# Kernel tuning notes

Hardware: AMD Instinct MI355X
Metric: run time of the kernel (lower is better)

## Reference

```python
import jax, jax.numpy as jnp
import numpy as np

B, N1, D, H = 64, 201, 128, 4
HALF = (N1 - 1) // 2  # 100 pickup/delivery pairs
V_RANGE = 6.0
NEG = -1e20


def _uni(key, shape):
    s = 1.0 / np.sqrt(shape[-1])
    return jax.random.uniform(key, shape, jnp.float32, -s, s)


def setup_inputs() -> dict:
    key = jax.random.key(0)
    ks = jax.random.split(key, 24)
    h_wave = jax.random.normal(ks[0], (B, N1, D), jnp.float32)
    # solution must be a valid permutation per batch (it is argsorted / self-gathered)
    solution = jax.vmap(lambda k: jax.random.permutation(k, N1))(jax.random.split(ks[1], B)).astype(jnp.int32)
    selection_recent = jax.random.uniform(ks[2], (B, 4, HALF), jnp.float32)
    pre_action = jax.random.randint(ks[3], (B, 2), 1, HALF).astype(jnp.int32)
    mask_table = jnp.zeros((B, N1, N1), dtype=bool)
    params = dict(
        Wn=_uni(ks[4], (D, D)), Wg=_uni(ks[5], (D, D)),
        rm_WQ=_uni(ks[6], (H, D, D)), rm_WK=_uni(ks[7], (H, D, D)),
        rm_w1=_uni(ks[8], (2 * H + 4, 32)), rm_b1=_uni(ks[9], (32,)),
        rm_w2=_uni(ks[10], (32, 32)), rm_b2=_uni(ks[11], (32,)),
        rm_w3=_uni(ks[12], (32, 1)), rm_b3=_uni(ks[13], (1,)),
        i1_Wq=_uni(ks[14], (H, D, D)), i1_Wk=_uni(ks[15], (H, D, D)),
        i2_Wq=_uni(ks[16], (H, D, D)), i2_Wk=_uni(ks[17], (H, D, D)),
        re_w1=_uni(ks[18], (4 * H, 32)), re_b1=_uni(ks[19], (32,)),
        re_w2=_uni(ks[20], (32, 32)), re_b2=_uni(ks[21], (32,)),
        re_w3=_uni(ks[22], (32, 1)), re_b3=_uni(ks[23], (1,)),
    )
    return dict(h_wave=h_wave, solution=solution, selection_recent=selection_recent,
                pre_action=pre_action, mask_table=mask_table, **params)


def _mlp(x, w1, b1, w2, b2, w3, b3):
    x = jax.nn.relu(x @ w1 + b1)
    x = jax.nn.relu(x @ w2 + b2)
    return (x @ w3 + b3)[..., 0]


def _mha_compat(q, k, Wq, Wk):
    # q: [B,Q,Din], k: [B,K,Din]; Wq/Wk: [H,Din,Dh] -> compat [H,B,Q,K]
    Q = jnp.einsum('bqd,hde->hbqe', q, Wq)
    K = jnp.einsum('bkd,hde->hbke', k, Wk)
    return jnp.einsum('hbqe,hbke->hbqk', Q, K) * (1.0 / np.sqrt(Wq.shape[-1]))


def _removal(h_hat, solution, selection_recent, WQ, WK, w1, b1, w2, b2, w3, b3):
    pre = jnp.argsort(solution, axis=1)
    post = jnp.take_along_axis(solution, solution, axis=1)
    hQ = jnp.einsum('bnd,hde->hbne', h_hat, WQ)  # [H,B,N1,D]
    hK = jnp.einsum('bnd,hde->hbne', h_hat, WK)
    Qpre = jnp.take_along_axis(hQ, pre[None, :, :, None], axis=2)
    Kpost = jnp.take_along_axis(hK, post[None, :, :, None], axis=2)
    comp = ((Qpre * hK).sum(-1) + (hQ * Kpost).sum(-1) - (Qpre * Kpost).sum(-1))[:, :, 1:]  # [H,B,N1-1]
    pairing = jnp.concatenate([comp[:, :, :N1 // 2], comp[:, :, N1 // 2:]], axis=0)  # [2H,B,HALF]
    feat = jnp.concatenate([jnp.transpose(pairing, (1, 2, 0)),
                            jnp.transpose(selection_recent, (0, 2, 1))], axis=-1)  # [B,HALF,2H+4]
    return _mlp(feat, w1, b1, w2, b2, w3, b3)  # [B,HALF]


def _reinsertion(h_hat, pos_pickup, pos_delivery, solution, Wq1, Wk1, Wq2, Wk2, w1, b1, w2, b2, w3, b3):
    ar = jnp.arange(B)
    h_p = h_hat[ar, pos_pickup][:, None, :]   # [B,1,D]
    h_d = h_hat[ar, pos_delivery][:, None, :]
    h_nb = jnp.take_along_axis(h_hat, solution[:, :, None], axis=1)  # [B,N1,D]

    def as_row(c):  # [H,B,1,N1] -> [B,N1,1,H] broadcast over columns
        return jnp.broadcast_to(jnp.transpose(c, (1, 2, 3, 0)).reshape(B, N1, 1, H), (B, N1, N1, H))

    def as_col(c):  # [H,B,1,N1] -> [B,1,N1,H] broadcast over rows
        return jnp.broadcast_to(jnp.transpose(c, (1, 2, 3, 0)).reshape(B, 1, N1, H), (B, N1, N1, H))

    feat = jnp.concatenate([
        as_row(_mha_compat(h_p, h_hat, Wq1, Wk1)),
        as_row(_mha_compat(h_p, h_nb, Wq2, Wk2)),
        as_col(_mha_compat(h_d, h_hat, Wq1, Wk1)),
        as_col(_mha_compat(h_d, h_nb, Wq2, Wk2)),
    ], axis=-1)  # [B,N1,N1,4H]
    return _mlp(feat, w1, b1, w2, b2, w3, b3)  # [B,N1,N1]


def _forward(h_wave, selection_recent, Wn, Wg, rm_WQ, rm_WK, rm_w1, rm_b1, rm_w2, rm_b2,
             rm_w3, rm_b3, i1_Wq, i1_Wk, i2_Wq, i2_Wk, re_w1, re_b1, re_w2, re_b2,
             re_w3, re_b3, solution, pre_action, mask_table):
    ar = jnp.arange(B)
    h_hat = h_wave @ Wn + (jnp.max(h_wave, axis=1) @ Wg)[:, None, :]
    t1 = jnp.tanh(_removal(h_hat, solution, selection_recent, rm_WQ, rm_WK,
                           rm_w1, rm_b1, rm_w2, rm_b2, rm_w3, rm_b3)) * V_RANGE
    t1 = jnp.where(pre_action[0, 0] > 0, t1.at[ar, pre_action[:, 0]].set(NEG), t1)
    logp1 = jax.nn.log_softmax(t1, axis=-1)
    a1 = jnp.argmax(t1, axis=-1)  # deterministic stand-in for Categorical sampling
    ll1 = jnp.take_along_axis(logp1, a1[:, None], axis=1)[:, 0]
    pos_pickup = 1 + a1
    pos_delivery = pos_pickup + HALF
    t2 = jnp.tanh(_reinsertion(h_hat, pos_pickup, pos_delivery, solution,
                               i1_Wq, i1_Wk, i2_Wq, i2_Wk,
                               re_w1, re_b1, re_w2, re_b2, re_w3, re_b3)) * V_RANGE
    t2 = jnp.where(mask_table, NEG, t2).reshape(B, N1 * N1)
    logp2 = jax.nn.log_softmax(t2, axis=-1)
    pair = jnp.argmax(t2, axis=-1)
    ll2 = jnp.take_along_axis(logp2, pair[:, None], axis=1)[:, 0]
    action = jnp.stack([a1, pair // N1, pair % N1], axis=-1)
    return action, ll1 + ll2


def reference(h_wave, solution, selection_recent, pre_action, mask_table,
              Wn, Wg, rm_WQ, rm_WK, rm_w1, rm_b1, rm_w2, rm_b2, rm_w3, rm_b3,
              i1_Wq, i1_Wk, i2_Wq, i2_Wk, re_w1, re_b1, re_w2, re_b2, re_w3, re_b3):
    return _forward(h_wave, selection_recent, Wn, Wg, rm_WQ, rm_WK, rm_w1, rm_b1,
                    rm_w2, rm_b2, rm_w3, rm_b3, i1_Wq, i1_Wk, i2_Wq, i2_Wk,
                    re_w1, re_b1, re_w2, re_b2, re_w3, re_b3,
                    solution, pre_action, mask_table)
```

## Files before the change

### kernel.cpp

```cpp
#include <hip/hip_runtime.h>
#include <math.h>

#define BB 64
#define N1 201
#define DD 128
#define HALF 100
#define NN (N1*N1)
#define NEGV (-1e20f)
#define QSCALE 0.08838834764831845f
#define NELE 1646592u

typedef __attribute__((ext_vector_type(8))) short short8v;
typedef __attribute__((ext_vector_type(4))) float float4v;

#define OFF_M    0u
#define OFF_MF   196608u
#define OFF_HWB  516096u
#define OFF_HHAT 2985984u
#define OFF_HBF  4632576u
#define OFF_G    7102464u
#define OFF_CMP  7110656u
#define OFF_Q    7161856u
#define OFF_ROWH 7292928u
#define OFF_COLH 7704576u
#define OFF_SC   8116224u
#define OFF_PM   8116480u
#define OFF_PS   8120576u
#define OFF_PI   8124672u
#define OFF_W2F  8128768u

__device__ __forceinline__ unsigned short f2bf(float x) {
    unsigned u = __float_as_uint(x);
    unsigned r = u + 0x7fffu + ((u >> 16) & 1u);
    return (unsigned short)(r >> 16);
}
__device__ __forceinline__ float bf2f(unsigned short h) {
    return __uint_as_float(((unsigned)h) << 16);
}

__global__ void kprep2(const float* __restrict__ rmWQ, const float* __restrict__ rmWK,
                       const float* __restrict__ i1Wq, const float* __restrict__ i1Wk,
                       const float* __restrict__ i2Wq, const float* __restrict__ i2Wk,
                       float* __restrict__ ws) {
    int m = blockIdx.x, ig = blockIdx.y, jg = blockIdx.z, t = threadIdx.x;
    const float* WQ; const float* WK;
    if (m < 4)      { WQ = rmWQ + m*16384;     WK = rmWK + m*16384; }
    else if (m < 8) { WQ = i1Wq + (m-4)*16384; WK = i1Wk + (m-4)*16384; }
    else            { WQ = i2Wq + (m-8)*16384; WK = i2Wk + (m-8)*16384; }
    __shared__ float wq[32*132];
    __shared__ float wk[32*133];
    for (int idx = t; idx < 32*128; idx += 128) {
        int r = idx >> 7, e = idx & 127;
        wq[r*132 + e] = WQ[(ig*32 + r)*128 + e];
        wk[r*133 + e] = WK[(jg*32 + r)*128 + e];
    }
    __syncthreads();
    int j = t & 31, iq = t >> 5;
    #pragma unroll
    for (int i2 = 0; i2 < 8; ++i2) {
        int i = iq*8 + i2;
        float acc = 0.f;
        #pragma unroll 8
        for (int e = 0; e < 128; ++e) acc += wq[i*132 + e]*wk[j*133 + e];
        ws[OFF_M + m*16384 + (ig*32 + i)*128 + jg*32 + j] = acc;
    }
}

__global__ void kfrag(const float* __restrict__ Wn, const float* __restrict__ re_w2,
                      float* __restrict__ ws) {
    int bid = blockIdx.x;
    int l = threadIdx.x;
    if (bid == 416) {
        unsigned short* w2f = (unsigned short*)(ws + OFF_W2F);
        for (int idx = l; idx < 2048; idx += 64) {
            int fs = idx >> 9, ll = (idx >> 3) & 63, i = idx & 7;
            int j = 16*(fs >> 1) + (ll & 15);
            int k = ((ll >> 4)*8) + i;
            float v = re_w2[k*32 + j];
            unsigned short hi = f2bf(v);
            w2f[idx] = (fs & 1) ? f2bf(v - bf2f(hi)) : hi;
        }
        return;
    }
    int mat = bid >> 5, rem = bid & 31, nt = rem >> 2, ks = rem & 3;
    const float* src = (mat < 12) ? (ws + OFF_M + mat*16384) : Wn;
    unsigned short* mf = (unsigned short*)(ws + OFF_MF)
                       + (size_t)mat*49152 + (size_t)((nt*4 + ks)*3)*512 + l*8;
    #pragma unroll
    for (int i = 0; i < 8; ++i) {
        int k = ks*32 + (l >> 4)*8 + i;
        int col = nt*16 + (l & 15);
        float v = src[k*128 + col];
        unsigned short h = f2bf(v);
        float r1 = v - bf2f(h);
        unsigned short mm = f2bf(r1);
        unsigned short lo = f2bf(r1 - bf2f(mm));
        mf[i] = h; mf[512 + i] = mm; mf[1024 + i] = lo;
    }
}

__global__ void khw3(const float* __restrict__ hw, float* __restrict__ ws) {
    unsigned idx = blockIdx.x*256u + threadIdx.x;
    if (idx >= NELE) return;
    unsigned short* hh = (unsigned short*)(ws + OFF_HWB);
    unsigned short* hm = hh + NELE;
    unsigned short* hl = hh + 2u*NELE;
    float v = hw[idx];
    unsigned short a = f2bf(v);
    float r1 = v - bf2f(a);
    unsigned short b = f2bf(r1);
    unsigned short c = f2bf(r1 - bf2f(b));
    hh[idx] = a; hm[idx] = b; hl[idx] = c;
}

__global__ void khmaxg2(const float* __restrict__ hw, const float* __restrict__ Wg,
                        float* __restrict__ g) {
    int b = blockIdx.x, d = threadIdx.x;
    __shared__ float hm[128];
    float m = -INFINITY;
    const float* src = hw + (size_t)b*N1*DD + d;
    for (int n = 0; n < N1; ++n) m = fmaxf(m, src[n*DD]);
    hm[d] = m;
    __syncthreads();
    float acc = 0.f;
    for (int k = 0; k < 128; ++k) acc += hm[k] * Wg[k*128 + d];
    g[b*128 + d] = acc;
}

__global__ __launch_bounds__(256) void khhat2(const float* __restrict__ g,
                                              float* __restrict__ ws) {
    int b = blockIdx.x, cg = blockIdx.y;
    int t = threadIdx.x, w = t >> 6, l = t & 63;
    const unsigned short* hwh = (const unsigned short*)(ws + OFF_HWB);
    const unsigned short* hwm = hwh + NELE;
    const unsigned short* hwl = hwh + 2u*NELE;
    const unsigned short* wnf = (const unsigned short*)(ws + OFF_MF) + (size_t)12*49152;
    float* hhat = ws + OFF_HHAT;
    unsigned short* hbh = (unsigned short*)(ws + OFF_HBF);
    unsigned short* hbm = hbh + NELE;
    unsigned short* hbl = hbh + 2u*NELE;
    int col0 = cg*32 + (l & 15);
    float g0 = g[b*128 + col0];
    float g1 = g[b*128 + col0 + 16];
    for (int mt = w; mt < 13; mt += 4) {
        int arow = mt*16 + (l & 15); if (arow > 200) arow = 200;
        size_t abase = ((size_t)b*N1 + arow)*DD;
        float4v acc0 = {g0, g0, g0, g0};
        float4v acc1 = {g1, g1, g1, g1};
        #pragma unroll
        for (int ks = 0; ks < 4; ++ks) {
            size_t ao = abase + ks*32 + (l >> 4)*8;
            short8v ah = *(const short8v*)(hwh + ao);
            short8v am = *(const short8v*)(hwm + ao);
            short8v al = *(const short8v*)(hwl + ao);
            const short8v* bf0 = (const short8v*)(wnf + (size_t)(((cg*2 + 0)*4 + ks)*3)*512) + l;
            const short8v* bf1 = (const short8v*)(wnf + (size_t)(((cg*2 + 1)*4 + ks)*3)*512) + l;
            short8v bh0 = bf0[0], bm0 = bf0[64], bl0 = bf0[128];
            short8v bh1 = bf1[0], bm1 = bf1[64], bl1 = bf1[128];
            acc0 = __builtin_amdgcn_mfma_f32_16x16x32_bf16(ah, bh0, acc0, 0, 0, 0);
            acc1 = __builtin_amdgcn_mfma_f32_16x16x32_bf16(ah, bh1, acc1, 0, 0, 0);
            acc0 = __builtin_amdgcn_mfma_f32_16x16x32_bf16(ah, bm0, acc0, 0, 0, 0);
            acc1 = __builtin_amdgcn_mfma_f32_16x16x32_bf16(ah, bm1, acc1, 0, 0, 0);
            acc0 = __builtin_amdgcn_mfma_f32_16x16x32_bf16(am, bh0, acc0, 0, 0, 0);
            acc1 = __builtin_amdgcn_mfma_f32_16x16x32_bf16(am, bh1, acc1, 0, 0, 0);
            acc0 = __builtin_amdgcn_mfma_f32_16x16x32_bf16(ah, bl0, acc0, 0, 0, 0);
            acc1 = __builtin_amdgcn_mfma_f32_16x16x32_bf16(ah, bl1, acc1, 0, 0, 0);
            acc0 = __builtin_amdgcn_mfma_f32_16x16x32_bf16(al, bh0, acc0, 0, 0, 0);
            acc1 = __builtin_amdgcn_mfma_f32_16x16x32_bf16(al, bh1, acc1, 0, 0, 0);
            acc0 = __builtin_amdgcn_mfma_f32_16x16x32_bf16(am, bm0, acc0, 0, 0, 0);
            acc1 = __builtin_amdgcn_mfma_f32_16x16x32_bf16(am, bm1, acc1, 0, 0, 0);
        }
        #pragma unroll
        for (int r = 0; r < 4; ++r) {
            int row = mt*16 + (l >> 4)*4 + r;
            if (row < N1) {
                size_t i0 = ((size_t)b*N1 + row)*DD + col0;
                float v0 = acc0[r], v1 = acc1[r];
                hhat[i0] = v0; hhat[i0 + 16] = v1;
                unsigned short a0 = f2bf(v0); float r10 = v0 - bf2f(a0);
                unsigned short b0 = f2bf(r10);
                hbh[i0] = a0; hbm[i0] = b0; hbl[i0] = f2bf(r10 - bf2f(b0));
                unsigned short a1 = f2bf(v1); float r11 = v1 - bf2f(a1);
                unsigned short b1 = f2bf(r11);
                hbh[i0+16] = a1; hbm[i0+16] = b1; hbl[i0+16] = f2bf(r11 - bf2f(b1));
            }
        }
    }
}

__global__ __launch_bounds__(256) void kAC(const int* __restrict__ solution,
                                           float* __restrict__ ws) {
    int b = blockIdx.x, h = blockIdx.y;
    int t = threadIdx.x, w = t >> 6, l = t & 63;
    __shared__ float As[N1*132];
    __shared__ int sol[N1], pre[N1], post[N1];
    if (t < N1) sol[t] = solution[b*N1 + t];
    __syncthreads();
    if (t < N1) { pre[sol[t]] = t; post[t] = sol[sol[t]]; }
    const unsigned short* hbh = (const unsigned short*)(ws + OFF_HBF);
    const unsigned short* hbm = hbh + NELE;
    const unsigned short* hbl = hbh + 2u*NELE;
    const unsigned short* mfm = (const unsigned short*)(ws + OFF_MF) + (size_t)h*49152;
    for (int mt = 0; mt < 13; ++mt) {
        int arow = mt*16 + (l & 15); if (arow > 200) arow = 200;
        size_t abase = ((size_t)b*N1 + arow)*DD;
        float4v acc0 = {0.f, 0.f, 0.f, 0.f};
        float4v acc1 = {0.f, 0.f, 0.f, 0.f};
        #pragma unroll
        for (int ks = 0; ks < 4; ++ks) {
            size_t ao = abase + ks*32 + (l >> 4)*8;
            short8v ah = *(const short8v*)(hbh + ao);
            short8v am = *(const short8v*)(hbm + ao);
            short8v al = *(const short8v*)(hbl + ao);
            const short8v* bf0 = (const short8v*)(mfm + (size_t)(((2*w + 0)*4 + ks)*3)*512) + l;
            const short8v* bf1 = (const short8v*)(mfm + (size_t)(((2*w + 1)*4 + ks)*3)*512) + l;
            short8v bh0 = bf0[0], bm0 = bf0[64], bl0 = bf0[128];
            short8v bh1 = bf1[0], bm1 = bf1[64], bl1 = bf1[128];
            acc0 = __builtin_amdgcn_mfma_f32_16x16x32_bf16(ah, bh0, acc0, 0, 0, 0);
            acc1 = __builtin_amdgcn_mfma_f32_16x16x32_bf16(ah, bh1, acc1, 0, 0, 0);
            acc0 = __builtin_amdgcn_mfma_f32_16x16x32_bf16(ah, bm0, acc0, 0, 0, 0);
            acc1 = __builtin_amdgcn_mfma_f32_16x16x32_bf16(ah, bm1, acc1, 0, 0, 0);
            acc0 = __builtin_amdgcn_mfma_f32_16x16x32_bf16(am, bh0, acc0, 0, 0, 0);
            acc1 = __builtin_amdgcn_mfma_f32_16x16x32_bf16(am, bh1, acc1, 0, 0, 0);
            acc0 = __builtin_amdgcn_mfma_f32_16x16x32_bf16(ah, bl0, acc0, 0, 0, 0);
            acc1 = __builtin_amdgcn_mfma_f32_16x16x32_bf16(ah, bl1, acc1, 0, 0, 0);
            acc0 = __builtin_amdgcn_mfma_f32_16x16x32_bf16(al, bh0, acc0, 0, 0, 0);
            acc1 = __builtin_amdgcn_mfma_f32_16x16x32_bf16(al, bh1, acc1, 0, 0, 0);
            acc0 = __builtin_amdgcn_mfma_f32_16x16x32_bf16(am, bm0, acc0, 0, 0, 0);
            acc1 = __builtin_amdgcn_mfma_f32_16x16x32_bf16(am, bm1, acc1, 0, 0, 0);
        }
        #pragma unroll
        for (int r = 0; r < 4; ++r) {
            int row = mt*16 + (l >> 4)*4 + r;
            if (row < N1) {
                int col = 2*w*16 + (l & 15);
                As[row*132 + col] = acc0[r];
                As[row*132 + col + 16] = acc1[r];
            }
        }
    }
    __syncthreads();
    const float2* X = (const float2*)(ws + OFF_HHAT) + (size_t)b*N1*64;
    float* cmp = ws + OFF_CMP + (h*64 + b)*200;
    for (int n = 1 + w; n <= 200; n += 4) {
        int pn = pre[n], po = post[n];
        float2 xn = X[n*64 + l], xp = X[po*64 + l];
        float2 ap = *(const float2*)&As[pn*132 + 2*l];
        float2 an = *(const float2*)&As[n*132 + 2*l];
        float v = ap.x*(xn.x - xp.x) + ap.y*(xn.y - xp.y) + an.x*xp.x + an.y*xp.y;
        #pragma unroll
        for (int off = 32; off; off >>= 1) v += __shfl_xor(v, off);
        if (l == 0) cmp[n - 1] = v;
    }
}

__global__ void krmq(const float* __restrict__ sel, const int* __restrict__ pre_action,
                     const float* __restrict__ w1, const float* __restrict__ b1,
                     const float* __restrict__ w2, const float* __restrict__ b2,
                     const float* __restrict__ w3, const float* __restrict__ b3,
                     const float* __restrict__ Mall, const float* __restrict__ hhat,
                     const float* __restrict__ cmpg, float* __restrict__ sc,
                     float* __restrict__ q) {
    int b = blockIdx.x, t = threadIdx.x;
    __shared__ float t1l[100];
    __shared__ int ppd[2];
    __shared__ float xp[128], xd[128];
    if (t < 100) {
        float f[12];
        #pragma unroll
        for (int h = 0; h < 4; ++h) {
            f[h]     = cmpg[(h*64 + b)*200 + t];
            f[4 + h] = cmpg[(h*64 + b)*200 + 100 + t];
        }
        #pragma unroll
        for (int s = 0; s < 4; ++s) f[8 + s] = sel[b*400 + s*100 + t];
        float h1[32];
        #pragma unroll
        for (int k = 0; k < 32; ++k) h1[k] = b1[k];
        #pragma unroll
        for (int j = 0; j < 12; ++j) {
            const float* wr = w1 + j*32;
            #pragma unroll
            for (int k = 0; k < 32; ++k) h1[k] += f[j]*wr[k];
        }
        #pragma unroll
        for (int k = 0; k < 32; ++k) h1[k] = fmaxf(h1[k], 0.f);
        float acc[32];
        #pragma unroll
        for (int j = 0; j < 32; ++j) acc[j] = b2[j];
        #pragma unroll
        for (int k = 0; k < 32; ++k) {
            const float* wr = w2 + k*32;
            #pragma unroll
            for (int j = 0; j < 32; ++j) acc[j] += h1[k]*wr[j];
        }
        float out = b3[0];
        #pragma unroll
        for (int j = 0; j < 32; ++j) out += fmaxf(acc[j], 0.f)*w3[j];
        t1l[t] = tanhf(out)*6.0f;
    }
    __syncthreads();
    if (t == 0) {
        if (pre_action[0] > 0) t1l[pre_action[b*2]] = NEGV;
        float M = -INFINITY; int a1 = 0;
        for (int i = 0; i < 100; ++i) if (t1l[i] > M) { M = t1l[i]; a1 = i; }
        float S = 0.f;
        for (int i = 0; i < 100; ++i) S += __expf(t1l[i] - M);
        int* ia = (int*)sc;
        ia[b] = a1;
        sc[192 + b] = -__logf(S);
        ppd[0] = 1 + a1; ppd[1] = 101 + a1;
    }
    __syncthreads();
    int pp = ppd[0], pd = ppd[1];
    const float* hb = hhat + (size_t)b*N1*DD;
    xp[t] = hb[pp*DD + t];
    xd[t] = hb[pd*DD + t];
    __syncthreads();
    int j = t;
    #pragma unroll
    for (int h = 0; h < 4; ++h) {
        const float* M1 = Mall + (4 + h)*16384;
        const float* M2 = Mall + (8 + h)*16384;
        float a1p = 0, a2p = 0, a1d = 0, a2d = 0;
        for (int i = 0; i < 128; ++i) {
            float w1v = M1[i*128 + j], w2v = M2[i*128 + j];
            a1p += xp[i]*w1v; a1d += xd[i]*w1v;
            a2p += xp[i]*w2v; a2d += xd[i]*w2v;
        }
        q[((0*4 + h)*64 + b)*128 + j] = a1p*QSCALE;
        q[((1*4 + h)*64 + b)*128 + j] = a2p*QSCALE;
        q[((2*4 + h)*64 + b)*128 + j] = a1d*QSCALE;
        q[((3*4 + h)*64 + b)*128 + j] = a2d*QSCALE;
    }
}

__global__ void krowcol(const int* __restrict__ solution, const float* __restrict__ w1,
                        const float* __restrict__ b1, const float* __restrict__ qg,
                        const float* __restrict__ hhat, float* __restrict__ rowH,
                        float* __restrict__ colH) {
    int b = blockIdx.x, ch = blockIdx.y, t = threadIdx.x;
    int n = ch*51 + t;
    int ne = ch*51 + 51; if (ne > N1) ne = N1;
    if (n >= ne || t >= 51) return;
    int sn = solution[b*N1 + n];
    const float* ra = hhat + ((size_t)b*N1 + n)*DD;
    const float* rb = hhat + ((size_t)b*N1 + sn)*DD;
    float cv[16];
    #pragma unroll
    for (int j = 0; j < 16; ++j) cv[j] = 0.f;
    for (int ec = 0; ec < 4; ++ec) {
        float xa[32], xb[32];
        #pragma unroll
        for (int q4 = 0; q4 < 8; ++q4) {
            float4 va = ((const float4*)(ra + ec*32))[q4];
            float4 vb = ((const float4*)(rb + ec*32))[q4];
            xa[q4*4+0]=va.x; xa[q4*4+1]=va.y; xa[q4*4+2]=va.z; xa[q4*4+3]=va.w;
            xb[q4*4+0]=vb.x; xb[q4*4+1]=vb.y; xb[q4*4+2]=vb.z; xb[q4*4+3]=vb.w;
        }
        #pragma unroll
        for (int j = 0; j < 16; ++j) {
            const float* qp = qg + ((size_t)j*64 + b)*128 + ec*32;
            int kind = j >> 2;
            float a = 0.f;
            if (kind & 1) {
                #pragma unroll
                for (int e = 0; e < 32; ++e) a += qp[e]*xb[e];
            } else {
                #pragma unroll
                for (int e = 0; e < 32; ++e) a += qp[e]*xa[e];
            }
            cv[j] += a;
        }
    }
    float* rO = rowH + ((size_t)b*N1 + n)*32;
    float* cO = colH + ((size_t)b*N1 + n)*32;
    #pragma unroll
    for (int k = 0; k < 32; ++k) {
        float rh = b1[k], chh = 0.f;
        #pragma unroll
        for (int j = 0; j < 8; ++j)  rh  += cv[j]*w1[j*32 + k];
        #pragma unroll
        for (int j = 8; j < 16; ++j) chh += cv[j]*w1[j*32 + k];
        rO[k] = rh; cO[k] = chh;
    }
}

__global__ __launch_bounds__(64) void kt2(
        const unsigned char* __restrict__ maskt,
        const float* __restrict__ rowH, const float* __restrict__ colH,
        const unsigned short* __restrict__ w2f,
        const float* __restrict__ b2g, const float* __restrict__ w3g,
        const float* __restrict__ b3g,
        float* __restrict__ pm, float* __restrict__ ps, int* __restrict__ pi) {
    int b = blockIdx.x, cy = blockIdx.y, rz = blockIdx.z;
    int l = threadIdx.x;
    int c0 = cy*64;
    int r0 = rz*13, rend = r0 + 13; if (rend > N1) rend = N1;
    int rcnt = rend - r0;
    __shared__ float colc[64*36];
    __shared__ float rowr[13*36];

    const short8v* wf = (const short8v*)w2f;
    short8v w2hi0 = wf[0*64 + l];
    short8v w2lo0 = wf[1*64 + l];
    short8v w2hi1 = wf[2*64 + l];
    short8v w2lo1 = wf[3*64 + l];
    int sg = l >> 4;
    float4v b2f0 = *(const float4v*)(b2g + sg*4);
    float4v b2f1 = *(const float4v*)(b2g + 16 + sg*4);
    float4v w3f0 = *(const float4v*)(w3g + sg*4);
    float4v w3f1 = *(const float4v*)(w3g + 16 + sg*4);
    float b3v = b3g[0];

    {
        int cg = c0 + l;
        float4v* dst = (float4v*)(colc + l*36);
        if (cg < N1) {
            const float4v* src = (const float4v*)(colH + ((size_t)b*N1 + cg)*32);
            #pragma unroll
            for (int q = 0; q < 8; ++q) dst[q] = src[q];
        } else {
            float4v z = {0.f, 0.f, 0.f, 0.f};
            #pragma unroll
            for (int q = 0; q < 8; ++q) dst[q] = z;
        }
    }
    for (int idx = l; idx < rcnt*32; idx += 64) {
        int rr = idx >> 5, k = idx & 31;
        rowr[rr*36 + k] = rowH[((size_t)b*N1 + r0 + rr)*32 + k];
    }
    __syncthreads();

    float m = -INFINITY, s = 0.f;
    int mi = 0x7fffffff;
    int c = c0 + l;
    bool valid = c < N1;
    const unsigned char* mrow = maskt + (size_t)b*NN + c0 + l;

    union U8 { unsigned u[4]; short8v s8; };

    for (int rr = 0; rr < rcnt; ++rr) {
        int r = r0 + rr;
        const float4v* rp = (const float4v*)(rowr + rr*36 + sg*8);
        float4v ra = rp[0], rb = rp[1];
        float outv = 0.f;
        #pragma unroll
        for (int g = 0; g < 4; ++g) {
            const float4v* cp = (const float4v*)(colc + (16*g + (l & 15))*36 + sg*8);
            float4v ca = cp[0], cb = cp[1];
            float h[8];
            #pragma unroll
            for (int e = 0; e < 4; ++e) {
                h[e]   = fmaxf(ra[e] + ca[e], 0.f);
                h[4+e] = fmaxf(rb[e] + cb[e], 0.f);
            }
            U8 B, L;
            #pragma unroll
            for (int e = 0; e < 4; ++e) {
                unsigned ph, pl;
                asm("v_cvt_pk_bf16_f32 %0, %1, %2" : "=v"(ph) : "v"(h[2*e]), "v"(h[2*e+1]));
                float h0 = __uint_as_float(ph << 16);
                float h1f = __uint_as_float(ph & 0xffff0000u);
                float l0 = h[2*e] - h0, l1 = h[2*e+1] - h1f;
                asm("v_cvt_pk_bf16_f32 %0, %1, %2" : "=v"(pl) : "v"(l0), "v"(l1));
                B.u[e] = ph; L.u[e] = pl;
            }
            short8v bh = B.s8, bl = L.s8;
            float4v a0 = b2f0, a1 = b2f1;
            a0 = __builtin_amdgcn_mfma_f32_16x16x32_bf16(w2hi0, bh, a0, 0, 0, 0);
            a0 = __builtin_amdgcn_mfma_f32_16x16x32_bf16(w2hi0, bl, a0, 0, 0, 0);
            a0 = __builtin_amdgcn_mfma_f32_16x16x32_bf16(w2lo0, bh, a0, 0, 0, 0);
            a0 = __builtin_amdgcn_mfma_f32_16x16x32_bf16(w2lo0, bl, a0, 0, 0, 0);
            a1 = __builtin_amdgcn_mfma_f32_16x16x32_bf16(w2hi1, bh, a1, 0, 0, 0);
            a1 = __builtin_amdgcn_mfma_f32_16x16x32_bf16(w2hi1, bl, a1, 0, 0, 0);
            a1 = __builtin_amdgcn_mfma_f32_16x16x32_bf16(w2lo1, bh, a1, 0, 0, 0);
            a1 = __builtin_amdgcn_mfma_f32_16x16x32_bf16(w2lo1, bl, a1, 0, 0, 0);
            float p = 0.f;
            #pragma unroll
            for (int reg = 0; reg < 4; ++reg) {
                p += fmaxf(a0[reg], 0.f)*w3f0[reg];
                p += fmaxf(a1[reg], 0.f)*w3f1[reg];
            }
            p += __shfl_xor(p, 16);
            p += __shfl_xor(p, 32);
            if (sg == g) outv = p + b3v;
        }
        float ex = __expf(2.f*outv);
        float tv = 6.f - 12.f/(ex + 1.f);
        if (mrow[(size_t)r*N1]) tv = NEGV;
        if (valid) {
            if (tv > m) { s = s*__expf(m - tv) + 1.f; m = tv; mi = r*N1 + c; }
            else        { s += __expf(tv - m); }
        }
    }
    #pragma unroll
    for (int off = 1; off < 64; off <<= 1) {
        float om = __shfl_xor(m, off);
        float os = __shfl_xor(s, off);
        int oi = __shfl_xor(mi, off);
        float M2 = fmaxf(m, om);
        float sn = (s > 0.f ? s*__expf(m - M2) : 0.f)
                 + (os > 0.f ? os*__expf(om - M2) : 0.f);
        int in_;
        if (m > om) in_ = mi; else if (om > m) in_ = oi; else in_ = (mi < oi ? mi : oi);
        m = M2; s = sn; mi = in_;
    }
    if (l == 0) {
        int slot = b*64 + cy*16 + rz;
        pm[slot] = m; ps[slot] = s; pi[slot] = mi;
    }
}

__global__ void kfinal(float* __restrict__ out, const float* __restrict__ pm,
                       const float* __restrict__ ps, const int* __restrict__ pi,
                       const float* __restrict__ sc) {
    int b = blockIdx.x, lane = threadIdx.x;
    float m = pm[b*64 + lane];
    float s = ps[b*64 + lane];
    int mi = pi[b*64 + lane];
    #pragma unroll
    for (int off = 1; off < 64; off <<= 1) {
        float om = __shfl_xor(m, off);
        float os = __shfl_xor(s, off);
        int oi = __shfl_xor(mi, off);
        float M2 = fmaxf(m, om);
        float sn = (s > 0.f ? s*__expf(m - M2) : 0.f)
                 + (os > 0.f ? os*__expf(om - M2) : 0.f);
        int in_;
        if (m > om) in_ = mi; else if (om > m) in_ = oi; else in_ = (mi < oi ? mi : oi);
        m = M2; s = sn; mi = in_;
    }
    if (lane == 0) {
        float ll2 = -__logf(s);
        const int* ia = (const int*)sc;
        out[b*3 + 0] = (float)ia[b];
        out[b*3 + 1] = (float)(mi / N1);
        out[b*3 + 2] = (float)(mi % N1);
        out[192 + b] = sc[192 + b] + ll2;
    }
}

extern "C" void kernel_launch(void* const* d_in, const int* in_sizes, int n_in,
                              void* d_out, int out_size, void* d_ws, size_t ws_size,
                              hipStream_t stream) {
    const float* h_wave    = (const float*)d_in[0];
    const int*   solution  = (const int*)d_in[1];
    const float* sel       = (const float*)d_in[2];
    const int*   pre_act   = (const int*)d_in[3];
    const unsigned char* maskt = (const unsigned char*)d_in[4];
    const float* Wn    = (const float*)d_in[5];
    const float* Wg    = (const float*)d_in[6];
    const float* rmWQ  = (const float*)d_in[7];
    const float* rmWK  = (const float*)d_in[8];
    const float* rm_w1 = (const float*)d_in[9];
    const float* rm_b1 = (const float*)d_in[10];
    const float* rm_w2 = (const float*)d_in[11];
    const float* rm_b2 = (const float*)d_in[12];
    const float* rm_w3 = (const float*)d_in[13];
    const float* rm_b3 = (const float*)d_in[14];
    const float* i1Wq  = (const float*)d_in[15];
    const float* i1Wk  = (const float*)d_in[16];
    const float* i2Wq  = (const float*)d_in[17];
    const float* i2Wk  = (const float*)d_in[18];
    const float* re_w1 = (const float*)d_in[19];
    const float* re_b1 = (const float*)d_in[20];
    const float* re_w2 = (const float*)d_in[21];
    const float* re_b2 = (const float*)d_in[22];
    const float* re_w3 = (const float*)d_in[23];
    const float* re_b3 = (const float*)d_in[24];
    float* ws = (float*)d_ws;
    float* out = (float*)d_out;

    kprep2<<<dim3(12, 4, 4), dim3(128), 0, stream>>>(rmWQ, rmWK, i1Wq, i1Wk, i2Wq, i2Wk, ws);
    kfrag<<<dim3(417), dim3(64), 0, stream>>>(Wn, re_w2, ws);
    khw3<<<dim3(6432), dim3(256), 0, stream>>>(h_wave, ws);
    khmaxg2<<<dim3(64), dim3(128), 0, stream>>>(h_wave, Wg, ws + OFF_G);
    khhat2<<<dim3(64, 4), dim3(256), 0, stream>>>(ws + OFF_G, ws);
    kAC<<<dim3(64, 4), dim3(256), 0, stream>>>(solution, ws);
    krmq<<<dim3(64), dim3(128), 0, stream>>>(sel, pre_act, rm_w1, rm_b1, rm_w2, rm_b2,
                                             rm_w3, rm_b3, ws + OFF_M, ws + OFF_HHAT,
                                             ws + OFF_CMP, ws + OFF_SC, ws + OFF_Q);
    krowcol<<<dim3(64, 4), dim3(64), 0, stream>>>(solution, re_w1, re_b1,
                                                  ws + OFF_Q, ws + OFF_HHAT,
                                                  ws + OFF_ROWH, ws + OFF_COLH);
    kt2<<<dim3(64, 4, 16), dim3(64), 0, stream>>>(maskt, ws + OFF_ROWH, ws + OFF_COLH,
                                                  (const unsigned short*)(ws + OFF_W2F),
                                                  re_b2, re_w3, re_b3,
                                                  ws + OFF_PM, ws + OFF_PS,
                                                  (int*)(ws + OFF_PI));
    kfinal<<<dim3(64), dim3(64), 0, stream>>>(out, ws + OFF_PM, ws + OFF_PS,
                                              (const int*)(ws + OFF_PI), ws + OFF_SC);
}
```

Before: 354.5 us.

## Move reinsertion row/col projections to split-bf16 MFMA and restructure kt2 blocks

The q vectors are stored as three-way bf16 splits, and the scalar krowcol kernel is replaced by krowcol2. krowcol2 computes the 16 q·h dot products with MFMA, using hi/mid/lo split products, then applies w1 from shared memory. kt2 now runs 4 waves per block, keeps column features in registers and prefetches row features instead of staging them in LDS. kt2 also drops the lo×lo MFMA term, trading a little precision for fewer MFMAs. The split-bf16 scheme approximates fp32 accuracy with extra loads and MFMA work.

```diff
diff --git a/kernel.cpp b/kernel.cpp
--- a/kernel.cpp
+++ b/kernel.cpp
@@ -20,7 +20,6 @@
 #define OFF_HBF  4632576u
 #define OFF_G    7102464u
 #define OFF_CMP  7110656u
-#define OFF_Q    7161856u
 #define OFF_ROWH 7292928u
 #define OFF_COLH 7704576u
 #define OFF_SC   8116224u
@@ -28,6 +27,7 @@
 #define OFF_PS   8120576u
 #define OFF_PI   8124672u
 #define OFF_W2F  8128768u
+#define OFF_QS   8130816u
 
 __device__ __forceinline__ unsigned short f2bf(float x) {
     unsigned u = __float_as_uint(x);
@@ -260,7 +260,7 @@
                      const float* __restrict__ w3, const float* __restrict__ b3,
                      const float* __restrict__ Mall, const float* __restrict__ hhat,
                      const float* __restrict__ cmpg, float* __restrict__ sc,
-                     float* __restrict__ q) {
+                     unsigned short* __restrict__ qs) {
     int b = blockIdx.x, t = threadIdx.x;
     __shared__ float t1l[100];
     __shared__ int ppd[2];
@@ -318,6 +318,9 @@
     xd[t] = hb[pd*DD + t];
     __syncthreads();
     int j = t;
+    unsigned short* qsh = qs;
+    unsigned short* qsm = qs + 131072;
+    unsigned short* qsl = qs + 262144;
     #pragma unroll
     for (int h = 0; h < 4; ++h) {
         const float* M1 = Mall + (4 + h)*16384;
@@ -328,65 +331,101 @@
             a1p += xp[i]*w1v; a1d += xd[i]*w1v;
             a2p += xp[i]*w2v; a2d += xd[i]*w2v;
         }
-        q[((0*4 + h)*64 + b)*128 + j] = a1p*QSCALE;
-        q[((1*4 + h)*64 + b)*128 + j] = a2p*QSCALE;
-        q[((2*4 + h)*64 + b)*128 + j] = a1d*QSCALE;
-        q[((3*4 + h)*64 + b)*128 + j] = a2d*QSCALE;
-    }
-}
-
-__global__ void krowcol(const int* __restrict__ solution, const float* __restrict__ w1,
-                        const float* __restrict__ b1, const float* __restrict__ qg,
-                        const float* __restrict__ hhat, float* __restrict__ rowH,
-                        float* __restrict__ colH) {
-    int b = blockIdx.x, ch = blockIdx.y, t = threadIdx.x;
-    int n = ch*51 + t;
-    int ne = ch*51 + 51; if (ne > N1) ne = N1;
-    if (n >= ne || t >= 51) return;
-    int sn = solution[b*N1 + n];
-    const float* ra = hhat + ((size_t)b*N1 + n)*DD;
-    const float* rb = hhat + ((size_t)b*N1 + sn)*DD;
-    float cv[16];
+        float vals[4] = {a1p*QSCALE, a2p*QSCALE, a1d*QSCALE, a2d*QSCALE};
+        #pragma unroll
+        for (int ty = 0; ty < 4; ++ty) {
+            size_t o = ((size_t)(ty*4 + h)*64 + b)*128 + j;
+            float v = vals[ty];
+            unsigned short hi = f2bf(v); float r1 = v - bf2f(hi);
+            unsigned short md = f2bf(r1);
+            qsh[o] = hi; qsm[o] = md; qsl[o] = f2bf(r1 - bf2f(md));
+        }
+    }
+}
+
+__global__ __launch_bounds__(256) void krowcol2(const int* __restrict__ sol_g,
+                                                const float* __restrict__ w1,
+                                                const float* __restrict__ b1,
+                                                float* __restrict__ ws) {
+    int b = blockIdx.x, zb = blockIdx.y;
+    int t = threadIdx.x, w = t >> 6, l = t & 63;
+    __shared__ int sol[N1];
+    __shared__ float carr[N1*17];
+    __shared__ float w1s[512];
+    __shared__ float b1s[32];
+    if (t < N1) sol[t] = sol_g[b*N1 + t];
+    for (int i = t; i < 512; i += 256) w1s[i] = w1[i];
+    if (t < 32) b1s[t] = b1[t];
+    __syncthreads();
+    const unsigned short* qsh = (const unsigned short*)(ws + OFF_QS);
+    const unsigned short* qsm = qsh + 131072;
+    const unsigned short* qsl = qsh + 262144;
+    const unsigned short* hbh = (const unsigned short*)(ws + OFF_HBF);
+    const unsigned short* hbm = hbh + NELE;
+    const unsigned short* hbl = hbh + 2u*NELE;
+    int j = l & 15;
+    short8v Bh[4], Bm[4], Bl[4];
     #pragma unroll
-    for (int j = 0; j < 16; ++j) cv[j] = 0.f;
-    for (int ec = 0; ec < 4; ++ec) {
-        float xa[32], xb[32];
-        #pragma unroll
-        for (int q4 = 0; q4 < 8; ++q4) {
-            float4 va = ((const float4*)(ra + ec*32))[q4];
-            float4 vb = ((const float4*)(rb + ec*32))[q4];
-            xa[q4*4+0]=va.x; xa[q4*4+1]=va.y; xa[q4*4+2]=va.z; xa[q4*4+3]=va.w;
-            xb[q4*4+0]=vb.x; xb[q4*4+1]=vb.y; xb[q4*4+2]=vb.z; xb[q4*4+3]=vb.w;
-        }
-        #pragma unroll
-        for (int j = 0; j < 16; ++j) {
-            const float* qp = qg + ((size_t)j*64 + b)*128 + ec*32;
-            int kind = j >> 2;
-            float a = 0.f;
-            if (kind & 1) {
-                #pragma unroll
-                for (int e = 0; e < 32; ++e) a += qp[e]*xb[e];
-            } else {
-                #pragma unroll
-                for (int e = 0; e < 32; ++e) a += qp[e]*xa[e];
-            }
-            cv[j] += a;
-        }
-    }
-    float* rO = rowH + ((size_t)b*N1 + n)*32;
-    float* cO = colH + ((size_t)b*N1 + n)*32;
-    #pragma unroll
-    for (int k = 0; k < 32; ++k) {
-        float rh = b1[k], chh = 0.f;
-        #pragma unroll
-        for (int j = 0; j < 8; ++j)  rh  += cv[j]*w1[j*32 + k];
-        #pragma unroll
-        for (int j = 8; j < 16; ++j) chh += cv[j]*w1[j*32 + k];
-        rO[k] = rh; cO[k] = chh;
-    }
-}
-
-__global__ __launch_bounds__(64) void kt2(
+    for (int ks = 0; ks < 4; ++ks) {
+        size_t qo = ((size_t)j*64 + b)*128 + ks*32 + (l >> 4)*8;
+        Bh[ks] = *(const short8v*)(qsh + qo);
+        Bm[ks] = *(const short8v*)(qsm + qo);
+        Bl[ks] = *(const short8v*)(qsl + qo);
+    }
+    int mt0 = zb ? 7 : 0, mt1 = zb ? 13 : 7;
+    for (int mt = mt0 + w; mt < mt1; mt += 4) {
+        int rA = mt*16 + j; if (rA > 200) rA = 200;
+        int rB = sol[rA];
+        size_t o1 = ((size_t)b*N1 + rA)*DD;
+        size_t o2 = ((size_t)b*N1 + rB)*DD;
+        float4v acc1 = {0.f, 0.f, 0.f, 0.f};
+        float4v acc2 = {0.f, 0.f, 0.f, 0.f};
+        #pragma unroll
+        for (int ks = 0; ks < 4; ++ks) {
+            size_t k0 = ks*32 + (l >> 4)*8;
+            short8v a1h = *(const short8v*)(hbh + o1 + k0);
+            short8v a1m = *(const short8v*)(hbm + o1 + k0);
+            short8v a1l = *(const short8v*)(hbl + o1 + k0);
+            acc1 = __builtin_amdgcn_mfma_f32_16x16x32_bf16(a1h, Bh[ks], acc1, 0, 0, 0);
+            acc1 = __builtin_amdgcn_mfma_f32_16x16x32_bf16(a1h, Bm[ks], acc1, 0, 0, 0);
+            acc1 = __builtin_amdgcn_mfma_f32_16x16x32_bf16(a1m, Bh[ks], acc1, 0, 0, 0);
+            acc1 = __builtin_amdgcn_mfma_f32_16x16x32_bf16(a1h, Bl[ks], acc1, 0, 0, 0);
+            acc1 = __builtin_amdgcn_mfma_f32_16x16x32_bf16(a1l, Bh[ks], acc1, 0, 0, 0);
+            acc1 = __builtin_amdgcn_mfma_f32_16x16x32_bf16(a1m, Bm[ks], acc1, 0, 0, 0);
+            short8v a2h = *(const short8v*)(hbh + o2 + k0);
+            short8v a2m = *(const short8v*)(hbm + o2 + k0);
+            short8v a2l = *(const short8v*)(hbl + o2 + k0);
+            acc2 = __builtin_amdgcn_mfma_f32_16x16x32_bf16(a2h, Bh[ks], acc2, 0, 0, 0);
+            acc2 = __builtin_amdgcn_mfma_f32_16x16x32_bf16(a2h, Bm[ks], acc2, 0, 0, 0);
+            acc2 = __builtin_amdgcn_mfma_f32_16x16x32_bf16(a2m, Bh[ks], acc2, 0, 0, 0);
+            acc2 = __builtin_amdgcn_mfma_f32_16x16x32_bf16(a2h, Bl[ks], acc2, 0, 0, 0);
+            acc2 = __builtin_amdgcn_mfma_f32_16x16x32_bf16(a2l, Bh[ks], acc2, 0, 0, 0);
+            acc2 = __builtin_amdgcn_mfma_f32_16x16x32_bf16(a2m, Bm[ks], acc2, 0, 0, 0);
+        }
+        int kodd = (j >> 2) & 1;
+        #pragma unroll
+        for (int r = 0; r < 4; ++r) {
+            int row = mt*16 + (l >> 4)*4 + r;
+            if (row < N1) carr[row*17 + j] = kodd ? acc2[r] : acc1[r];
+        }
+    }
+    __syncthreads();
+    int rows0 = zb*112, nrows = zb ? 89 : 112;
+    float* rowH = ws + OFF_ROWH;
+    float* colH = ws + OFF_COLH;
+    for (int idx = t; idx < nrows*32; idx += 256) {
+        int n = rows0 + (idx >> 5), k = idx & 31;
+        float rh = b1s[k], ch = 0.f;
+        #pragma unroll
+        for (int jj = 0; jj < 8; ++jj)  rh += carr[n*17 + jj]*w1s[jj*32 + k];
+        #pragma unroll
+        for (int jj = 8; jj < 16; ++jj) ch += carr[n*17 + jj]*w1s[jj*32 + k];
+        rowH[((size_t)b*N1 + n)*32 + k] = rh;
+        colH[((size_t)b*N1 + n)*32 + k] = ch;
+    }
+}
+
+__global__ __launch_bounds__(256) void kt2(
         const unsigned char* __restrict__ maskt,
         const float* __restrict__ rowH, const float* __restrict__ colH,
         const unsigned short* __restrict__ w2f,
@@ -394,66 +433,52 @@
         const float* __restrict__ b3g,
         float* __restrict__ pm, float* __restrict__ ps, int* __restrict__ pi) {
     int b = blockIdx.x, cy = blockIdx.y, rz = blockIdx.z;
-    int l = threadIdx.x;
+    int t = threadIdx.x, w = t >> 6, l = t & 63;
     int c0 = cy*64;
-    int r0 = rz*13, rend = r0 + 13; if (rend > N1) rend = N1;
-    int rcnt = rend - r0;
-    __shared__ float colc[64*36];
-    __shared__ float rowr[13*36];
-
+    int sg = l >> 4;
     const short8v* wf = (const short8v*)w2f;
     short8v w2hi0 = wf[0*64 + l];
     short8v w2lo0 = wf[1*64 + l];
     short8v w2hi1 = wf[2*64 + l];
     short8v w2lo1 = wf[3*64 + l];
-    int sg = l >> 4;
     float4v b2f0 = *(const float4v*)(b2g + sg*4);
     float4v b2f1 = *(const float4v*)(b2g + 16 + sg*4);
     float4v w3f0 = *(const float4v*)(w3g + sg*4);
     float4v w3f1 = *(const float4v*)(w3g + 16 + sg*4);
     float b3v = b3g[0];
-
-    {
-        int cg = c0 + l;
-        float4v* dst = (float4v*)(colc + l*36);
-        if (cg < N1) {
-            const float4v* src = (const float4v*)(colH + ((size_t)b*N1 + cg)*32);
-            #pragma unroll
-            for (int q = 0; q < 8; ++q) dst[q] = src[q];
-        } else {
-            float4v z = {0.f, 0.f, 0.f, 0.f};
-            #pragma unroll
-            for (int q = 0; q < 8; ++q) dst[q] = z;
-        }
-    }
-    for (int idx = l; idx < rcnt*32; idx += 64) {
-        int rr = idx >> 5, k = idx & 31;
-        rowr[rr*36 + k] = rowH[((size_t)b*N1 + r0 + rr)*32 + k];
-    }
-    __syncthreads();
-
+    float4v ca[4], cb[4];
+    #pragma unroll
+    for (int g = 0; g < 4; ++g) {
+        int cc = c0 + 16*g + (l & 15); if (cc > 200) cc = 200;
+        const float4v* cp = (const float4v*)(colH + ((size_t)b*N1 + cc)*32 + sg*8);
+        ca[g] = cp[0]; cb[g] = cp[1];
+    }
+    int r0 = rz*52 + w*13;
+    int c = c0 + l;
+    bool cvalid = c < N1;
+    int cS = cvalid ? c : 200;
     float m = -INFINITY, s = 0.f;
     int mi = 0x7fffffff;
-    int c = c0 + l;
-    bool valid = c < N1;
-    const unsigned char* mrow = maskt + (size_t)b*NN + c0 + l;
-
+    const float* rbase = rowH + (size_t)b*N1*32 + sg*8;
     union U8 { unsigned u[4]; short8v s8; };
-
-    for (int rr = 0; rr < rcnt; ++rr) {
+    int rl0 = r0 > 200 ? 200 : r0;
+    float4v ra = ((const float4v*)(rbase + (size_t)rl0*32))[0];
+    float4v rb = ((const float4v*)(rbase + (size_t)rl0*32))[1];
+    for (int rr = 0; rr < 13; ++rr) {
         int r = r0 + rr;
-        const float4v* rp = (const float4v*)(rowr + rr*36 + sg*8);
-        float4v ra = rp[0], rb = rp[1];
+        int rn = r + 1; if (rn > 200) rn = 200;
+        const float4v* rpn = (const float4v*)(rbase + (size_t)rn*32);
+        float4v ra_n = rpn[0], rb_n = rpn[1];
+        int rS = r > 200 ? 200 : r;
+        unsigned char mv = maskt[(size_t)b*NN + (size_t)rS*N1 + cS];
         float outv = 0.f;
         #pragma unroll
         for (int g = 0; g < 4; ++g) {
-            const float4v* cp = (const float4v*)(colc + (16*g + (l & 15))*36 + sg*8);
-            float4v ca = cp[0], cb = cp[1];
             float h[8];
             #pragma unroll
             for (int e = 0; e < 4; ++e) {
-                h[e]   = fmaxf(ra[e] + ca[e], 0.f);
-                h[4+e] = fmaxf(rb[e] + cb[e], 0.f);
+                h[e]   = fmaxf(ra[e] + ca[g][e], 0.f);
+                h[4+e] = fmaxf(rb[e] + cb[g][e], 0.f);
             }
             U8 B, L;
             #pragma unroll
@@ -466,16 +491,13 @@
                 asm("v_cvt_pk_bf16_f32 %0, %1, %2" : "=v"(pl) : "v"(l0), "v"(l1));
                 B.u[e] = ph; L.u[e] = pl;
             }
-            short8v bh = B.s8, bl = L.s8;
             float4v a0 = b2f0, a1 = b2f1;
-            a0 = __builtin_amdgcn_mfma_f32_16x16x32_bf16(w2hi0, bh, a0, 0, 0, 0);
-            a0 = __builtin_amdgcn_mfma_f32_16x16x32_bf16(w2hi0, bl, a0, 0, 0, 0);
-            a0 = __builtin_amdgcn_mfma_f32_16x16x32_bf16(w2lo0, bh, a0, 0, 0, 0);
-            a0 = __builtin_amdgcn_mfma_f32_16x16x32_bf16(w2lo0, bl, a0, 0, 0, 0);
-            a1 = __builtin_amdgcn_mfma_f32_16x16x32_bf16(w2hi1, bh, a1, 0, 0, 0);
-            a1 = __builtin_amdgcn_mfma_f32_16x16x32_bf16(w2hi1, bl, a1, 0, 0, 0);
-            a1 = __builtin_amdgcn_mfma_f32_16x16x32_bf16(w2lo1, bh, a1, 0, 0, 0);
-            a1 = __builtin_amdgcn_mfma_f32_16x16x32_bf16(w2lo1, bl, a1, 0, 0, 0);
+            a0 = __builtin_amdgcn_mfma_f32_16x16x32_bf16(w2hi0, B.s8, a0, 0, 0, 0);
+            a1 = __builtin_amdgcn_mfma_f32_16x16x32_bf16(w2hi1, B.s8, a1, 0, 0, 0);
+            a0 = __builtin_amdgcn_mfma_f32_16x16x32_bf16(w2hi0, L.s8, a0, 0, 0, 0);
+            a1 = __builtin_amdgcn_mfma_f32_16x16x32_bf16(w2hi1, L.s8, a1, 0, 0, 0);
+            a0 = __builtin_amdgcn_mfma_f32_16x16x32_bf16(w2lo0, B.s8, a0, 0, 0, 0);
+            a1 = __builtin_amdgcn_mfma_f32_16x16x32_bf16(w2lo1, B.s8, a1, 0, 0, 0);
             float p = 0.f;
             #pragma unroll
             for (int reg = 0; reg < 4; ++reg) {
@@ -486,10 +508,11 @@
             p += __shfl_xor(p, 32);
             if (sg == g) outv = p + b3v;
         }
+        ra = ra_n; rb = rb_n;
         float ex = __expf(2.f*outv);
         float tv = 6.f - 12.f/(ex + 1.f);
-        if (mrow[(size_t)r*N1]) tv = NEGV;
-        if (valid) {
+        if (mv) tv = NEGV;
+        if ((r < N1) && cvalid) {
             if (tv > m) { s = s*__expf(m - tv) + 1.f; m = tv; mi = r*N1 + c; }
             else        { s += __expf(tv - m); }
         }
@@ -507,7 +530,7 @@
         m = M2; s = sn; mi = in_;
     }
     if (l == 0) {
-        int slot = b*64 + cy*16 + rz;
+        int slot = b*64 + cy*16 + rz*4 + w;
         pm[slot] = m; ps[slot] = s; pi[slot] = mi;
     }
 }
@@ -580,11 +603,10 @@
     kAC<<<dim3(64, 4), dim3(256), 0, stream>>>(solution, ws);
     krmq<<<dim3(64), dim3(128), 0, stream>>>(sel, pre_act, rm_w1, rm_b1, rm_w2, rm_b2,
                                              rm_w3, rm_b3, ws + OFF_M, ws + OFF_HHAT,
-                                             ws + OFF_CMP, ws + OFF_SC, ws + OFF_Q);
-    krowcol<<<dim3(64, 4), dim3(64), 0, stream>>>(solution, re_w1, re_b1,
-                                                  ws + OFF_Q, ws + OFF_HHAT,
-                                                  ws + OFF_ROWH, ws + OFF_COLH);
-    kt2<<<dim3(64, 4, 16), dim3(64), 0, stream>>>(maskt, ws + OFF_ROWH, ws + OFF_COLH,
+                                             ws + OFF_CMP, ws + OFF_SC,
+                                             (unsigned short*)(ws + OFF_QS));
+    krowcol2<<<dim3(64, 2), dim3(256), 0, stream>>>(solution, re_w1, re_b1, ws);
+    kt2<<<dim3(64, 4, 4), dim3(256), 0, stream>>>(maskt, ws + OFF_ROWH, ws + OFF_COLH,
                                                   (const unsigned short*)(ws + OFF_W2F),
                                                   re_b2, re_w3, re_b3,
                                                   ws + OFF_PM, ws + OFF_PS,
```

Result: faster. 318.3 us (-10.2%).
